# Optimization experiments

Hardware: AMD Instinct MI355X
Metric: run time of the kernel (lower is better)

Reference implementation:

```python
import jax, jax.numpy as jnp
import numpy as np

B, S, D_IN, D_OUT, H = 4, 2048, 1024, 1024, 16
HD = D_OUT // H

def setup_inputs() -> dict:
    key = jax.random.key(0)
    ks = jax.random.split(key, 6)
    s = 1.0 / np.sqrt(D_IN)
    return {
        "x": jax.random.normal(ks[0], (B, S, D_IN), dtype=jnp.float32),
        "Wq": jax.random.uniform(ks[1], (D_IN, D_OUT), jnp.float32, -s, s),
        "Wk": jax.random.uniform(ks[2], (D_IN, D_OUT), jnp.float32, -s, s),
        "Wv": jax.random.uniform(ks[3], (D_IN, D_OUT), jnp.float32, -s, s),
        "Wo": jax.random.uniform(ks[4], (D_OUT, D_OUT), jnp.float32, -s, s),
        "bo": jax.random.uniform(ks[5], (D_OUT,), jnp.float32, -s, s),
    }

def reference(x, Wq, Wk, Wv, Wo, bo):
    b, n, _ = x.shape
    # project and split heads: [b, h, n, hd]
    q = (x @ Wq).reshape(b, n, H, HD).transpose(0, 2, 1, 3)
    k = (x @ Wk).reshape(b, n, H, HD).transpose(0, 2, 1, 3)
    v = (x @ Wv).reshape(b, n, H, HD).transpose(0, 2, 1, 3)
    scores = jnp.einsum("bhqd,bhkd->bhqk", q, k) / np.sqrt(HD).astype(np.float32)
    causal = jnp.tril(jnp.ones((n, n), dtype=bool))
    scores = jnp.where(causal, scores, -jnp.inf)
    attn = jax.nn.softmax(scores, axis=-1)  # dropout p=0.0 -> identity
    ctx = jnp.einsum("bhqk,bhkd->bhqd", attn, v)
    ctx = ctx.transpose(0, 2, 1, 3).reshape(b, n, D_OUT)
    return ctx @ Wo + bo
```

## Files before the change

### kernel.cpp

```cpp
#include <hip/hip_runtime.h>
#include <stdint.h>

#define B_   4
#define S_   2048
#define DI   1024
#define DOUT 1024
#define NHD  16
#define HD   64

typedef __attribute__((ext_vector_type(8))) short short8;
typedef __attribute__((ext_vector_type(4))) float f32x4;
typedef __attribute__((ext_vector_type(16))) float f32x16;

__device__ __forceinline__ unsigned short f32_bf16(float f) {
  union { float f; unsigned u; } v; v.f = f;
  unsigned r = v.u + 0x7FFFu + ((v.u >> 16) & 1u);
  return (unsigned short)(r >> 16);
}

__device__ __forceinline__ unsigned cvt_pk_bf16(float a, float b) {
  unsigned r;
  asm("v_cvt_pk_bf16_f32 %0, %1, %2" : "=v"(r) : "v"(a), "v"(b));
  return r;
}

__device__ __forceinline__ void pl32swap(unsigned &dst, unsigned &src) {
  asm("v_permlane32_swap_b32 %0, %1" : "+v"(dst), "+v"(src));
}

__device__ __forceinline__ float max3f(float a, float b, float c) {
  float d;
  asm("v_max3_f32 %0, %1, %2, %3" : "=v"(d) : "v"(a), "v"(b), "v"(c));
  return d;
}

__device__ __forceinline__ void gl_lds16(const void* g, void* s) {
  __builtin_amdgcn_global_load_lds(
      (const __attribute__((address_space(1))) unsigned int*)g,
      (__attribute__((address_space(3))) unsigned int*)s, 16, 0, 0);
}

#define EXP2(x) __builtin_amdgcn_exp2f(x)

__global__ __launch_bounds__(256) void cvt_kernel(const float* __restrict__ src,
                                                  unsigned short* __restrict__ dst, int n4) {
  int i = blockIdx.x * blockDim.x + threadIdx.x;
  if (i < n4) {
    float4 v = ((const float4*)src)[i];
    ushort4 o;
    o.x = f32_bf16(v.x); o.y = f32_bf16(v.y); o.z = f32_bf16(v.z); o.w = f32_bf16(v.w);
    ((ushort4*)dst)[i] = o;
  }
}

__global__ __launch_bounds__(256) void wtrans4_kernel(
    const float* __restrict__ W0, const float* __restrict__ W1,
    const float* __restrict__ W2, const float* __restrict__ W3,
    unsigned short* __restrict__ T0, unsigned short* __restrict__ T1,
    unsigned short* __restrict__ T2, unsigned short* __restrict__ T3) {
  __shared__ __attribute__((aligned(16))) float tile[64][65];
  const int z = blockIdx.z;
  const float* W = z == 0 ? W0 : z == 1 ? W1 : z == 2 ? W2 : W3;
  unsigned short* Wt = z == 0 ? T0 : z == 1 ? T1 : z == 2 ? T2 : T3;
  const int k0 = blockIdx.y * 64;
  const int n0 = blockIdx.x * 64;
  const int tid = threadIdx.x;
#pragma unroll
  for (int i = 0; i < 4; i++) {
    int c = tid + i * 256;
    int r = c >> 4;
    int cc = (c & 15) * 4;
    float4 v = *(const float4*)(W + (size_t)(k0 + r) * DOUT + n0 + cc);
    tile[r][cc] = v.x; tile[r][cc + 1] = v.y; tile[r][cc + 2] = v.z; tile[r][cc + 3] = v.w;
  }
  __syncthreads();
#pragma unroll
  for (int i = 0; i < 4; i++) {
    int c = tid + i * 256;
    int r = c >> 4;
    int cc = (c & 15) * 4;
    ushort4 o;
    o.x = f32_bf16(tile[cc + 0][r]);
    o.y = f32_bf16(tile[cc + 1][r]);
    o.z = f32_bf16(tile[cc + 2][r]);
    o.w = f32_bf16(tile[cc + 3][r]);
    *(ushort4*)(Wt + (size_t)(n0 + r) * DI + k0 + cc) = o;
  }
}

__device__ __forceinline__ int cswz(int r, int c) {
  return r * 128 + ((((c >> 3) ^ ((r >> 3) & 15)) << 3) | (c & 7));
}

template <int MODE>
__global__ __launch_bounds__(256) void gemm_kernel(
    const unsigned short* __restrict__ A,
    const unsigned short* __restrict__ Bt,
    unsigned short* __restrict__ oQ,
    unsigned short* __restrict__ oK,
    unsigned short* __restrict__ oV,
    float* __restrict__ outF,
    const float* __restrict__ bias,
    int M, int N, int K) {
  __shared__ __attribute__((aligned(16))) unsigned short smem[16384];
  const int tid = threadIdx.x;
  const int lane = tid & 63;
  const int w = tid >> 6;
  const int wm = w >> 1, wn = w & 1;
  const int quad = lane >> 4, l16 = lane & 15;
  const int m0 = blockIdx.x * 128;
  const int n0 = blockIdx.y * 128;

  const int lr = lane >> 2;
  const int lc8 = (lane & 3) * 8;
  const unsigned short* gA0 = A + (size_t)(m0 + w * 32 + lr) * K + lc8;
  const unsigned short* gA1 = gA0 + (size_t)16 * K;
  const unsigned short* gB0 = Bt + (size_t)(n0 + w * 32 + lr) * K + lc8;
  const unsigned short* gB1 = gB0 + (size_t)16 * K;
  const int sA0o = (w * 2 + 0) * 512;
  const int sA1o = (w * 2 + 1) * 512;
  const int sB0o = 4096 + (w * 2 + 0) * 512;
  const int sB1o = 4096 + (w * 2 + 1) * 512;

  f32x4 acc[4][4] = {};

  gl_lds16(gA0, smem + sA0o);
  gl_lds16(gA1, smem + sA1o);
  gl_lds16(gB0, smem + sB0o);
  gl_lds16(gB1, smem + sB1o);
  __syncthreads();

  for (int k0 = 0; k0 < K; k0 += 32) {
    const int cb = ((k0 >> 5) & 1) << 13;
    const int nb = 8192 - cb;
    if (k0 + 32 < K) {
      gl_lds16(gA0 + k0 + 32, smem + nb + sA0o);
      gl_lds16(gA1 + k0 + 32, smem + nb + sA1o);
      gl_lds16(gB0 + k0 + 32, smem + nb + sB0o);
      gl_lds16(gB1 + k0 + 32, smem + nb + sB1o);
    }
    short8 af[4], bfr[4];
#pragma unroll
    for (int mi = 0; mi < 4; mi++)
      af[mi] = *(const short8*)(smem + cb + (wm * 64 + mi * 16 + l16) * 32 + quad * 8);
#pragma unroll
    for (int ni = 0; ni < 4; ni++)
      bfr[ni] = *(const short8*)(smem + cb + 4096 + (wn * 64 + ni * 16 + l16) * 32 + quad * 8);
#pragma unroll
    for (int mi = 0; mi < 4; mi++)
#pragma unroll
      for (int ni = 0; ni < 4; ni++)
        acc[mi][ni] = __builtin_amdgcn_mfma_f32_16x16x32_bf16(af[mi], bfr[ni], acc[mi][ni], 0, 0, 0);
    __syncthreads();
  }

  if (MODE == 0) {
    const int which = n0 >> 10;
    if (which == 2) {
#pragma unroll
      for (int mi = 0; mi < 4; mi++)
#pragma unroll
        for (int ni = 0; ni < 4; ni++)
#pragma unroll
          for (int r = 0; r < 4; r++)
            smem[cswz(wm * 64 + mi * 16 + quad * 4 + r, wn * 64 + ni * 16 + l16)] =
                f32_bf16(acc[mi][ni][r]);
      __syncthreads();
      const int b = m0 >> 11, sb = m0 & 2047;
#pragma unroll
      for (int i = 0; i < 8; i++) {
        int c = tid + i * 256;
        int cl = c >> 4;
        int sc = (c & 15) * 8;
        int col = n0 + cl;
        int hh = (col >> 6) & 15, hd = col & 63;
        union { unsigned short u[8]; uint4 v; } t;
#pragma unroll
        for (int j = 0; j < 8; j++) t.u[j] = smem[cswz(sc + j, cl)];
        *(uint4*)(oV + (((size_t)(b * NHD + hh)) * HD + hd) * S_ + sb + sc) = t.v;
      }
    } else {
      unsigned short* dst0 = which == 0 ? oQ : oK;
#pragma unroll
      for (int mi = 0; mi < 4; mi++)
#pragma unroll
        for (int ni = 0; ni < 4; ni++) {
          const int col = n0 + wn * 64 + ni * 16 + l16;
          const int hh = (col >> 6) & 15, hd = col & 63;
#pragma unroll
          for (int r = 0; r < 4; r++) {
            const int row = m0 + wm * 64 + mi * 16 + quad * 4 + r;
            int b = row >> 11, s = row & 2047;
            dst0[(((size_t)(b * NHD + hh)) * S_ + s) * HD + hd] = f32_bf16(acc[mi][ni][r]);
          }
        }
    }
  } else {
#pragma unroll
    for (int mi = 0; mi < 4; mi++)
#pragma unroll
      for (int ni = 0; ni < 4; ni++) {
        const int col = n0 + wn * 64 + ni * 16 + l16;
        float bv = bias[col];
#pragma unroll
        for (int r = 0; r < 4; r++) {
          const int row = m0 + wm * 64 + mi * 16 + quad * 4 + r;
          outF[(size_t)row * N + col] = acc[mi][ni][r] + bv;
        }
      }
  }
}

__global__ __launch_bounds__(256, 2) void attn_kernel(
    const unsigned short* __restrict__ Q,
    const unsigned short* __restrict__ Kmat,
    const unsigned short* __restrict__ Vt,
    unsigned short* __restrict__ ctx) {
  __shared__ __attribute__((aligned(16))) unsigned short Ks[2][64 * 64];
  __shared__ __attribute__((aligned(16))) unsigned short Vs[2][64 * 64];
  __shared__ __attribute__((aligned(16))) unsigned short PsT[128 * 72];

  const int tid = threadIdx.x;
  const int lane = tid & 63;
  const int w = tid >> 6;
  const int l32 = lane & 31;
  const int h = lane >> 5;

  const int bh = blockIdx.x & 63;
  const int jj = blockIdx.x >> 6;

  const unsigned short* Qh = Q + (size_t)bh * S_ * HD;
  const unsigned short* Kh = Kmat + (size_t)bh * S_ * HD;
  const unsigned short* Vh = Vt + (size_t)bh * HD * S_;

  const int sr = tid >> 2;
  const int jA = tid & 3, jB = jA + 4;
  const int sswA = sr * 64 + ((jA ^ (sr & 7)) << 3);
  const int sswB = sr * 64 + ((jB ^ (sr & 7)) << 3);
  const unsigned short* gKA = Kh + (size_t)sr * HD + jA * 8;
  const unsigned short* gKB = Kh + (size_t)sr * HD + jB * 8;
  const unsigned short* gVA = Vh + (size_t)sr * S_ + jA * 8;
  const unsigned short* gVB = Vh + (size_t)sr * S_ + jB * 8;
  const int swz = (l32 & 7);

  unsigned short* myP = PsT + (size_t)(w * 32) * 72;
  const float scl = 0.18033688f;
  const int b = bh >> 4, head = bh & 15;

  for (int ph = 0; ph < 2; ph++) {
    const int qc = (ph == 0) ? (jj * 8 + w) : (63 - jj * 8 - w);
    const int nt = (qc >> 1) + 1;
    const int ntmax = (ph == 0) ? (jj * 4 + 2) : (32 - jj * 4);
    const int qrow = qc * 32 + l32;

    short8 qf[4];
#pragma unroll
    for (int ks = 0; ks < 4; ks++)
      qf[ks] = *(const short8*)(Qh + (size_t)qrow * HD + ks * 16 + h * 8);

    uint4 kregA = *(const uint4*)gKA, kregB = *(const uint4*)gKB;
    uint4 vregA = *(const uint4*)gVA, vregB = *(const uint4*)gVB;
    *(uint4*)(&Ks[0][sswA]) = kregA;
    *(uint4*)(&Ks[0][sswB]) = kregB;
    *(uint4*)(&Vs[0][sswA]) = vregA;
    *(uint4*)(&Vs[0][sswB]) = vregB;
    __syncthreads();

    f32x16 oacc[2] = {};
    float m_run = -__builtin_inff();
    float l_run = 0.f;

    for (int kt = 0; kt < ntmax; kt++) {
      if (kt + 1 < ntmax) {
        kregA = *(const uint4*)(gKA + (size_t)(kt + 1) * 64 * HD);
        kregB = *(const uint4*)(gKB + (size_t)(kt + 1) * 64 * HD);
        vregA = *(const uint4*)(gVA + (size_t)(kt + 1) * 64);
        vregB = *(const uint4*)(gVB + (size_t)(kt + 1) * 64);
      }
      const unsigned short* Kb_ = Ks[kt & 1];
      const unsigned short* Vb_ = Vs[kt & 1];

      if (kt < nt) {
        const int k0 = kt * 64;
        f32x16 sacc[2] = {};
#pragma unroll
        for (int ks = 0; ks < 4; ks++)
#pragma unroll
          for (int mi = 0; mi < 2; mi++) {
            short8 kf = *(const short8*)(Kb_ + (mi * 32 + l32) * 64 + (((ks * 2 + h) ^ swz) << 3));
            sacc[mi] = __builtin_amdgcn_mfma_f32_32x32x16_bf16(kf, qf[ks], sacc[mi], 0, 0, 0);
          }

        if (kt == nt - 1) {
#pragma unroll
          for (int mi = 0; mi < 2; mi++)
#pragma unroll
            for (int e = 0; e < 16; e++) {
              int key = k0 + mi * 32 + (e & 3) + 8 * (e >> 2) + 4 * h;
              if (key > qrow) sacc[mi][e] = -__builtin_inff();
            }
        }
        float vmax = fmaxf(sacc[0][0], sacc[0][1]);
#pragma unroll
        for (int e = 2; e < 16; e += 2) vmax = max3f(vmax, sacc[0][e], sacc[0][e + 1]);
#pragma unroll
        for (int e = 0; e < 16; e += 2) vmax = max3f(vmax, sacc[1][e], sacc[1][e + 1]);
        vmax = fmaxf(vmax, __shfl_xor(vmax, 32));
        const float pm = vmax * scl;
        if (!__all(pm <= m_run + 8.f)) {
          const float mnew = fmaxf(m_run, pm);
          const float alpha = EXP2(m_run - mnew);
          m_run = mnew;
          l_run *= alpha;
#pragma unroll
          for (int mi = 0; mi < 2; mi++) oacc[mi] *= alpha;
        }

        float rs = 0.f;
#pragma unroll
        for (int mi = 0; mi < 2; mi++)
#pragma unroll
          for (int e = 0; e < 16; e++) {
            float p = EXP2(fmaf(sacc[mi][e], scl, -m_run));
            sacc[mi][e] = p;
            rs += p;
          }
        rs += __shfl_xor(rs, 32);
        l_run += rs;

        short8 pfr[4];
#pragma unroll
        for (int mi = 0; mi < 2; mi++) {
          unsigned w0 = cvt_pk_bf16(sacc[mi][0], sacc[mi][1]);
          unsigned w1 = cvt_pk_bf16(sacc[mi][2], sacc[mi][3]);
          unsigned w2 = cvt_pk_bf16(sacc[mi][4], sacc[mi][5]);
          unsigned w3 = cvt_pk_bf16(sacc[mi][6], sacc[mi][7]);
          pl32swap(w0, w2);
          pl32swap(w1, w3);
          union { unsigned u[4]; short8 s; } lo;
          lo.u[0] = w0; lo.u[1] = w1; lo.u[2] = w2; lo.u[3] = w3;
          pfr[2 * mi + 0] = lo.s;
          unsigned x0 = cvt_pk_bf16(sacc[mi][8], sacc[mi][9]);
          unsigned x1 = cvt_pk_bf16(sacc[mi][10], sacc[mi][11]);
          unsigned x2 = cvt_pk_bf16(sacc[mi][12], sacc[mi][13]);
          unsigned x3 = cvt_pk_bf16(sacc[mi][14], sacc[mi][15]);
          pl32swap(x0, x2);
          pl32swap(x1, x3);
          union { unsigned u[4]; short8 s; } hi;
          hi.u[0] = x0; hi.u[1] = x1; hi.u[2] = x2; hi.u[3] = x3;
          pfr[2 * mi + 1] = hi.s;
        }

#pragma unroll
        for (int ks2 = 0; ks2 < 4; ks2++) {
#pragma unroll
          for (int mi2 = 0; mi2 < 2; mi2++) {
            short8 vf = *(const short8*)(Vb_ + (mi2 * 32 + l32) * 64 + (((ks2 * 2 + h) ^ swz) << 3));
            oacc[mi2] = __builtin_amdgcn_mfma_f32_32x32x16_bf16(vf, pfr[ks2], oacc[mi2], 0, 0, 0);
          }
        }
      }

      if (kt + 1 < ntmax) {
        *(uint4*)(&Ks[(kt + 1) & 1][sswA]) = kregA;
        *(uint4*)(&Ks[(kt + 1) & 1][sswB]) = kregB;
        *(uint4*)(&Vs[(kt + 1) & 1][sswA]) = vregA;
        *(uint4*)(&Vs[(kt + 1) & 1][sswB]) = vregB;
      }
      __syncthreads();
    }

    const float inv = 1.f / l_run;
#pragma unroll
    for (int mi2 = 0; mi2 < 2; mi2++)
#pragma unroll
      for (int g = 0; g < 4; g++) {
        uint2 pk;
        pk.x = cvt_pk_bf16(oacc[mi2][4 * g + 0] * inv, oacc[mi2][4 * g + 1] * inv);
        pk.y = cvt_pk_bf16(oacc[mi2][4 * g + 2] * inv, oacc[mi2][4 * g + 3] * inv);
        *(uint2*)(myP + l32 * 72 + mi2 * 32 + g * 8 + h * 4) = pk;
      }
#pragma unroll
    for (int p = 0; p < 4; p++) {
      int r = p * 8 + (lane >> 3);
      int c = (lane & 7) * 8;
      uint4 vv = *(const uint4*)(myP + r * 72 + c);
      *(uint4*)(ctx + ((size_t)(b * S_ + qc * 32 + r)) * DOUT + head * 64 + c) = vv;
    }
  }
}

extern "C" void kernel_launch(void* const* d_in, const int* in_sizes, int n_in,
                              void* d_out, int out_size, void* d_ws, size_t ws_size,
                              hipStream_t stream) {
  const float* x  = (const float*)d_in[0];
  const float* Wq = (const float*)d_in[1];
  const float* Wk = (const float*)d_in[2];
  const float* Wv = (const float*)d_in[3];
  const float* Wo = (const float*)d_in[4];
  const float* bo = (const float*)d_in[5];
  float* out = (float*)d_out;
  char* ws = (char*)d_ws;

  const size_t MB = 1024 * 1024;
  unsigned short* Wqt = (unsigned short*)(ws + 0 * MB);
  unsigned short* Wkt = (unsigned short*)(ws + 2 * MB);
  unsigned short* Wvt = (unsigned short*)(ws + 4 * MB);
  unsigned short* Wot = (unsigned short*)(ws + 6 * MB);
  unsigned short* xb  = (unsigned short*)(ws + 8 * MB);
  unsigned short* Qb  = (unsigned short*)(ws + 24 * MB);
  unsigned short* Kb  = (unsigned short*)(ws + 40 * MB);
  unsigned short* Vtb = (unsigned short*)(ws + 72 * MB);
  unsigned short* ctxb = xb;

  cvt_kernel<<<8192, 256, 0, stream>>>(x, xb, 2097152);
  wtrans4_kernel<<<dim3(16, 16, 4), 256, 0, stream>>>(Wq, Wk, Wv, Wo, Wqt, Wkt, Wvt, Wot);
  gemm_kernel<0><<<dim3(64, 24), 256, 0, stream>>>(xb, Wqt, Qb, Kb, Vtb, nullptr, nullptr,
                                                   8192, 3072, 1024);
  attn_kernel<<<512, 256, 0, stream>>>(Qb, Kb, Vtb, ctxb);
  gemm_kernel<1><<<dim3(64, 8), 256, 0, stream>>>(ctxb, Wot, nullptr, nullptr, nullptr, out, bo,
                                                  8192, 1024, 1024);
}
```

Baseline: 238.9 us.

## Switch projection GEMM to 32x32x16 MFMA with two-tile-ahead prefetch pipeline

The projection and output GEMM kernel now uses 32x32x16 bf16 MFMA tiles (2x2 per wave) in place of 16x16x32 tiles (4x4 per wave). This cuts the number of LDS fragment reads per MFMA FLOP. The K loop is restructured to keep two tiles in flight, with explicit vmcnt/lgkmcnt waits and raw s_barrier, so global-to-LDS loads overlap with compute. The epilogues are remapped to the 32x32 accumulator layout. The risk lies in correctness of the hand-placed waitcnt and barrier ordering, and the double buffer is reused right after fragments are read.

Result: slower. 246.0 us (+3.0%).

```diff
diff --git a/kernel.cpp b/kernel.cpp
--- a/kernel.cpp
+++ b/kernel.cpp
@@ -107,7 +107,8 @@
   const int lane = tid & 63;
   const int w = tid >> 6;
   const int wm = w >> 1, wn = w & 1;
-  const int quad = lane >> 4, l16 = lane & 15;
+  const int l32 = lane & 31;
+  const int h = lane >> 5;
   const int m0 = blockIdx.x * 128;
   const int n0 = blockIdx.y * 128;
 
@@ -122,49 +123,68 @@
   const int sB0o = 4096 + (w * 2 + 0) * 512;
   const int sB1o = 4096 + (w * 2 + 1) * 512;
 
-  f32x4 acc[4][4] = {};
-
-  gl_lds16(gA0, smem + sA0o);
-  gl_lds16(gA1, smem + sA1o);
-  gl_lds16(gB0, smem + sB0o);
-  gl_lds16(gB1, smem + sB1o);
-  __syncthreads();
-
-  for (int k0 = 0; k0 < K; k0 += 32) {
-    const int cb = ((k0 >> 5) & 1) << 13;
-    const int nb = 8192 - cb;
-    if (k0 + 32 < K) {
-      gl_lds16(gA0 + k0 + 32, smem + nb + sA0o);
-      gl_lds16(gA1 + k0 + 32, smem + nb + sA1o);
-      gl_lds16(gB0 + k0 + 32, smem + nb + sB0o);
-      gl_lds16(gB1 + k0 + 32, smem + nb + sB1o);
+  f32x16 acc[2][2] = {};
+
+  const int nt = K >> 5;
+
+#define STAGE_T(t, bufS)                                \
+  do {                                                  \
+    gl_lds16(gA0 + (t) * 32, smem + (bufS) + sA0o);     \
+    gl_lds16(gA1 + (t) * 32, smem + (bufS) + sA1o);     \
+    gl_lds16(gB0 + (t) * 32, smem + (bufS) + sB0o);     \
+    gl_lds16(gB1 + (t) * 32, smem + (bufS) + sB1o);     \
+  } while (0)
+
+  STAGE_T(0, 0);
+  STAGE_T(1, 8192);
+  asm volatile("s_waitcnt vmcnt(4)" ::: "memory");
+  __builtin_amdgcn_s_barrier();
+
+  for (int it = 0; it < nt; ++it) {
+    const int cb = (it & 1) << 13;
+    short8 af[2][2], bf[2][2];
+#pragma unroll
+    for (int mi = 0; mi < 2; mi++)
+#pragma unroll
+      for (int ks = 0; ks < 2; ks++)
+        af[mi][ks] = *(const short8*)(smem + cb + (wm * 64 + mi * 32 + l32) * 32 + (ks * 2 + h) * 8);
+#pragma unroll
+    for (int ni = 0; ni < 2; ni++)
+#pragma unroll
+      for (int ks = 0; ks < 2; ks++)
+        bf[ni][ks] = *(const short8*)(smem + cb + 4096 + (wn * 64 + ni * 32 + l32) * 32 + (ks * 2 + h) * 8);
+    asm volatile("s_waitcnt lgkmcnt(0)" ::: "memory");
+    __builtin_amdgcn_s_barrier();
+    if (it + 2 < nt) STAGE_T(it + 2, cb);
+#pragma unroll
+    for (int mi = 0; mi < 2; mi++)
+#pragma unroll
+      for (int ni = 0; ni < 2; ni++) {
+        acc[mi][ni] = __builtin_amdgcn_mfma_f32_32x32x16_bf16(af[mi][0], bf[ni][0], acc[mi][ni], 0, 0, 0);
+        acc[mi][ni] = __builtin_amdgcn_mfma_f32_32x32x16_bf16(af[mi][1], bf[ni][1], acc[mi][ni], 0, 0, 0);
+      }
+    if (it + 2 < nt) {
+      asm volatile("s_waitcnt vmcnt(4)" ::: "memory");
+    } else {
+      asm volatile("s_waitcnt vmcnt(0)" ::: "memory");
     }
-    short8 af[4], bfr[4];
-#pragma unroll
-    for (int mi = 0; mi < 4; mi++)
-      af[mi] = *(const short8*)(smem + cb + (wm * 64 + mi * 16 + l16) * 32 + quad * 8);
-#pragma unroll
-    for (int ni = 0; ni < 4; ni++)
-      bfr[ni] = *(const short8*)(smem + cb + 4096 + (wn * 64 + ni * 16 + l16) * 32 + quad * 8);
-#pragma unroll
-    for (int mi = 0; mi < 4; mi++)
-#pragma unroll
-      for (int ni = 0; ni < 4; ni++)
-        acc[mi][ni] = __builtin_amdgcn_mfma_f32_16x16x32_bf16(af[mi], bfr[ni], acc[mi][ni], 0, 0, 0);
-    __syncthreads();
-  }
+    __builtin_amdgcn_s_barrier();
+  }
+#undef STAGE_T
 
   if (MODE == 0) {
     const int which = n0 >> 10;
     if (which == 2) {
 #pragma unroll
-      for (int mi = 0; mi < 4; mi++)
-#pragma unroll
-        for (int ni = 0; ni < 4; ni++)
-#pragma unroll
-          for (int r = 0; r < 4; r++)
-            smem[cswz(wm * 64 + mi * 16 + quad * 4 + r, wn * 64 + ni * 16 + l16)] =
-                f32_bf16(acc[mi][ni][r]);
+      for (int mi = 0; mi < 2; mi++)
+#pragma unroll
+        for (int ni = 0; ni < 2; ni++)
+#pragma unroll
+          for (int e = 0; e < 16; e++) {
+            const int rw = (e & 3) + 8 * (e >> 2) + 4 * h;
+            smem[cswz(wm * 64 + mi * 32 + rw, wn * 64 + ni * 32 + l32)] =
+                f32_bf16(acc[mi][ni][e]);
+          }
       __syncthreads();
       const int b = m0 >> 11, sb = m0 & 2047;
 #pragma unroll
@@ -182,30 +202,30 @@
     } else {
       unsigned short* dst0 = which == 0 ? oQ : oK;
 #pragma unroll
-      for (int mi = 0; mi < 4; mi++)
-#pragma unroll
-        for (int ni = 0; ni < 4; ni++) {
-          const int col = n0 + wn * 64 + ni * 16 + l16;
+      for (int mi = 0; mi < 2; mi++)
+#pragma unroll
+        for (int ni = 0; ni < 2; ni++) {
+          const int col = n0 + wn * 64 + ni * 32 + l32;
           const int hh = (col >> 6) & 15, hd = col & 63;
 #pragma unroll
-          for (int r = 0; r < 4; r++) {
-            const int row = m0 + wm * 64 + mi * 16 + quad * 4 + r;
+          for (int e = 0; e < 16; e++) {
+            const int row = m0 + wm * 64 + mi * 32 + (e & 3) + 8 * (e >> 2) + 4 * h;
             int b = row >> 11, s = row & 2047;
-            dst0[(((size_t)(b * NHD + hh)) * S_ + s) * HD + hd] = f32_bf16(acc[mi][ni][r]);
+            dst0[(((size_t)(b * NHD + hh)) * S_ + s) * HD + hd] = f32_bf16(acc[mi][ni][e]);
           }
         }
     }
   } else {
 #pragma unroll
-    for (int mi = 0; mi < 4; mi++)
-#pragma unroll
-      for (int ni = 0; ni < 4; ni++) {
-        const int col = n0 + wn * 64 + ni * 16 + l16;
+    for (int mi = 0; mi < 2; mi++)
+#pragma unroll
+      for (int ni = 0; ni < 2; ni++) {
+        const int col = n0 + wn * 64 + ni * 32 + l32;
         float bv = bias[col];
 #pragma unroll
-        for (int r = 0; r < 4; r++) {
-          const int row = m0 + wm * 64 + mi * 16 + quad * 4 + r;
-          outF[(size_t)row * N + col] = acc[mi][ni][r] + bv;
+        for (int e = 0; e < 16; e++) {
+          const int row = m0 + wm * 64 + mi * 32 + (e & 3) + 8 * (e >> 2) + 4 * h;
+          outF[(size_t)row * N + col] = acc[mi][ni][e] + bv;
         }
       }
   }
```

## Process 64 query rows per wave in attention and remap blocks across XCDs

Applied to the files above, without the earlier changes.

Each attention wave now handles two 32-row query chunks (64 rows) against every K/V tile loaded into shared memory. This doubles the reuse of each K/V fragment read from LDS per MFMA and halves the number of blocks to 256. Block indices in both the GEMM and attention kernels are also remapped so that neighbouring tiles and heads land on the same XCD, aiming for better L2 locality. The trade-offs are roughly twice the accumulator and Q-fragment registers, which may hurt occupancy, and fewer blocks than before with coarser causal load balancing.

Result: slower. 256.4 us (+7.3%).

```diff
diff --git a/kernel.cpp b/kernel.cpp
--- a/kernel.cpp
+++ b/kernel.cpp
@@ -108,8 +108,14 @@
   const int w = tid >> 6;
   const int wm = w >> 1, wn = w & 1;
   const int quad = lane >> 4, l16 = lane & 15;
-  const int m0 = blockIdx.x * 128;
-  const int n0 = blockIdx.y * 128;
+
+  const int bid = blockIdx.y * 64 + blockIdx.x;
+  const int xcd = bid & 7;
+  const int rr = bid >> 3;
+  const int bx = xcd * 8 + (rr & 7);
+  const int by = rr >> 3;
+  const int m0 = bx * 128;
+  const int n0 = by * 128;
 
   const int lr = lane >> 2;
   const int lc8 = (lane & 3) * 8;
@@ -176,7 +182,7 @@
         int hh = (col >> 6) & 15, hd = col & 63;
         union { unsigned short u[8]; uint4 v; } t;
 #pragma unroll
-        for (int j = 0; j < 8; j++) t.u[j] = smem[cswz(sc + j, cl)];
+        for (int jx = 0; jx < 8; jx++) t.u[jx] = smem[cswz(sc + jx, cl)];
         *(uint4*)(oV + (((size_t)(b * NHD + hh)) * HD + hd) * S_ + sb + sc) = t.v;
       }
     } else {
@@ -226,8 +232,10 @@
   const int l32 = lane & 31;
   const int h = lane >> 5;
 
-  const int bh = blockIdx.x & 63;
-  const int jj = blockIdx.x >> 6;
+  const int bid = blockIdx.x;
+  const int bh = (bid & 7) * 8 + ((bid >> 3) & 7);
+  const int j = bid >> 6;
+  const int slot = 4 * j + w;
 
   const unsigned short* Qh = Q + (size_t)bh * S_ * HD;
   const unsigned short* Kh = Kmat + (size_t)bh * S_ * HD;
@@ -248,15 +256,17 @@
   const int b = bh >> 4, head = bh & 15;
 
   for (int ph = 0; ph < 2; ph++) {
-    const int qc = (ph == 0) ? (jj * 8 + w) : (63 - jj * 8 - w);
-    const int nt = (qc >> 1) + 1;
-    const int ntmax = (ph == 0) ? (jj * 4 + 2) : (32 - jj * 4);
-    const int qrow = qc * 32 + l32;
-
-    short8 qf[4];
-#pragma unroll
-    for (int ks = 0; ks < 4; ks++)
-      qf[ks] = *(const short8*)(Qh + (size_t)qrow * HD + ks * 16 + h * 8);
+    const int qp = (ph == 0) ? slot : (31 - slot);
+    const int nt = qp + 1;
+    const int ntmax = (ph == 0) ? (4 * j + 4) : (32 - 4 * j);
+    const int qr0 = qp * 64;
+
+    short8 qf[2][4];
+#pragma unroll
+    for (int c = 0; c < 2; c++)
+#pragma unroll
+      for (int ks = 0; ks < 4; ks++)
+        qf[c][ks] = *(const short8*)(Qh + (size_t)(qr0 + c * 32 + l32) * HD + ks * 16 + h * 8);
 
     uint4 kregA = *(const uint4*)gKA, kregB = *(const uint4*)gKB;
     uint4 vregA = *(const uint4*)gVA, vregB = *(const uint4*)gVB;
@@ -266,9 +276,9 @@
     *(uint4*)(&Vs[0][sswB]) = vregB;
     __syncthreads();
 
-    f32x16 oacc[2] = {};
-    float m_run = -__builtin_inff();
-    float l_run = 0.f;
+    f32x16 oacc[2][2] = {};
+    float m_run[2] = {-__builtin_inff(), -__builtin_inff()};
+    float l_run[2] = {0.f, 0.f};
 
     for (int kt = 0; kt < ntmax; kt++) {
       if (kt + 1 < ntmax) {
@@ -282,83 +292,92 @@
 
       if (kt < nt) {
         const int k0 = kt * 64;
-        f32x16 sacc[2] = {};
+        f32x16 sacc[2][2] = {};
 #pragma unroll
         for (int ks = 0; ks < 4; ks++)
 #pragma unroll
           for (int mi = 0; mi < 2; mi++) {
             short8 kf = *(const short8*)(Kb_ + (mi * 32 + l32) * 64 + (((ks * 2 + h) ^ swz) << 3));
-            sacc[mi] = __builtin_amdgcn_mfma_f32_32x32x16_bf16(kf, qf[ks], sacc[mi], 0, 0, 0);
+            sacc[0][mi] = __builtin_amdgcn_mfma_f32_32x32x16_bf16(kf, qf[0][ks], sacc[0][mi], 0, 0, 0);
+            sacc[1][mi] = __builtin_amdgcn_mfma_f32_32x32x16_bf16(kf, qf[1][ks], sacc[1][mi], 0, 0, 0);
           }
 
         if (kt == nt - 1) {
 #pragma unroll
+          for (int c = 0; c < 2; c++) {
+            const int qrow = qr0 + c * 32 + l32;
+#pragma unroll
+            for (int mi = 0; mi < 2; mi++)
+#pragma unroll
+              for (int e = 0; e < 16; e++) {
+                int key = k0 + mi * 32 + (e & 3) + 8 * (e >> 2) + 4 * h;
+                if (key > qrow) sacc[c][mi][e] = -__builtin_inff();
+              }
+          }
+        }
+
+        short8 pfr[2][4];
+#pragma unroll
+        for (int c = 0; c < 2; c++) {
+          float vmax = fmaxf(sacc[c][0][0], sacc[c][0][1]);
+#pragma unroll
+          for (int e = 2; e < 16; e += 2) vmax = max3f(vmax, sacc[c][0][e], sacc[c][0][e + 1]);
+#pragma unroll
+          for (int e = 0; e < 16; e += 2) vmax = max3f(vmax, sacc[c][1][e], sacc[c][1][e + 1]);
+          vmax = fmaxf(vmax, __shfl_xor(vmax, 32));
+          const float pm = vmax * scl;
+          if (!__all(pm <= m_run[c] + 8.f)) {
+            const float mnew = fmaxf(m_run[c], pm);
+            const float alpha = EXP2(m_run[c] - mnew);
+            m_run[c] = mnew;
+            l_run[c] *= alpha;
+#pragma unroll
+            for (int mi = 0; mi < 2; mi++) oacc[c][mi] *= alpha;
+          }
+
+          float rs = 0.f;
+#pragma unroll
           for (int mi = 0; mi < 2; mi++)
 #pragma unroll
             for (int e = 0; e < 16; e++) {
-              int key = k0 + mi * 32 + (e & 3) + 8 * (e >> 2) + 4 * h;
-              if (key > qrow) sacc[mi][e] = -__builtin_inff();
+              float p = EXP2(fmaf(sacc[c][mi][e], scl, -m_run[c]));
+              sacc[c][mi][e] = p;
+              rs += p;
             }
+          rs += __shfl_xor(rs, 32);
+          l_run[c] += rs;
+
+#pragma unroll
+          for (int mi = 0; mi < 2; mi++) {
+            unsigned w0 = cvt_pk_bf16(sacc[c][mi][0], sacc[c][mi][1]);
+            unsigned w1 = cvt_pk_bf16(sacc[c][mi][2], sacc[c][mi][3]);
+            unsigned w2 = cvt_pk_bf16(sacc[c][mi][4], sacc[c][mi][5]);
+            unsigned w3 = cvt_pk_bf16(sacc[c][mi][6], sacc[c][mi][7]);
+            pl32swap(w0, w2);
+            pl32swap(w1, w3);
+            union { unsigned u[4]; short8 s; } lo;
+            lo.u[0] = w0; lo.u[1] = w1; lo.u[2] = w2; lo.u[3] = w3;
+            pfr[c][2 * mi + 0] = lo.s;
+            unsigned x0 = cvt_pk_bf16(sacc[c][mi][8], sacc[c][mi][9]);
+            unsigned x1 = cvt_pk_bf16(sacc[c][mi][10], sacc[c][mi][11]);
+            unsigned x2 = cvt_pk_bf16(sacc[c][mi][12], sacc[c][mi][13]);
+            unsigned x3 = cvt_pk_bf16(sacc[c][mi][14], sacc[c][mi][15]);
+            pl32swap(x0, x2);
+            pl32swap(x1, x3);
+            union { unsigned u[4]; short8 s; } hi;
+            hi.u[0] = x0; hi.u[1] = x1; hi.u[2] = x2; hi.u[3] = x3;
+            pfr[c][2 * mi + 1] = hi.s;
+          }
         }
-        float vmax = fmaxf(sacc[0][0], sacc[0][1]);
-#pragma unroll
-        for (int e = 2; e < 16; e += 2) vmax = max3f(vmax, sacc[0][e], sacc[0][e + 1]);
-#pragma unroll
-        for (int e = 0; e < 16; e += 2) vmax = max3f(vmax, sacc[1][e], sacc[1][e + 1]);
-        vmax = fmaxf(vmax, __shfl_xor(vmax, 32));
-        const float pm = vmax * scl;
-        if (!__all(pm <= m_run + 8.f)) {
-          const float mnew = fmaxf(m_run, pm);
-          const float alpha = EXP2(m_run - mnew);
-          m_run = mnew;
-          l_run *= alpha;
-#pragma unroll
-          for (int mi = 0; mi < 2; mi++) oacc[mi] *= alpha;
-        }
-
-        float rs = 0.f;
-#pragma unroll
-        for (int mi = 0; mi < 2; mi++)
-#pragma unroll
-          for (int e = 0; e < 16; e++) {
-            float p = EXP2(fmaf(sacc[mi][e], scl, -m_run));
-            sacc[mi][e] = p;
-            rs += p;
-          }
-        rs += __shfl_xor(rs, 32);
-        l_run += rs;
-
-        short8 pfr[4];
-#pragma unroll
-        for (int mi = 0; mi < 2; mi++) {
-          unsigned w0 = cvt_pk_bf16(sacc[mi][0], sacc[mi][1]);
-          unsigned w1 = cvt_pk_bf16(sacc[mi][2], sacc[mi][3]);
-          unsigned w2 = cvt_pk_bf16(sacc[mi][4], sacc[mi][5]);
-          unsigned w3 = cvt_pk_bf16(sacc[mi][6], sacc[mi][7]);
-          pl32swap(w0, w2);
-          pl32swap(w1, w3);
-          union { unsigned u[4]; short8 s; } lo;
-          lo.u[0] = w0; lo.u[1] = w1; lo.u[2] = w2; lo.u[3] = w3;
-          pfr[2 * mi + 0] = lo.s;
-          unsigned x0 = cvt_pk_bf16(sacc[mi][8], sacc[mi][9]);
-          unsigned x1 = cvt_pk_bf16(sacc[mi][10], sacc[mi][11]);
-          unsigned x2 = cvt_pk_bf16(sacc[mi][12], sacc[mi][13]);
-          unsigned x3 = cvt_pk_bf16(sacc[mi][14], sacc[mi][15]);
-          pl32swap(x0, x2);
-          pl32swap(x1, x3);
-          union { unsigned u[4]; short8 s; } hi;
-          hi.u[0] = x0; hi.u[1] = x1; hi.u[2] = x2; hi.u[3] = x3;
-          pfr[2 * mi + 1] = hi.s;
-        }
-
-#pragma unroll
-        for (int ks2 = 0; ks2 < 4; ks2++) {
+
+#pragma unroll
+        for (int ks2 = 0; ks2 < 4; ks2++)
 #pragma unroll
           for (int mi2 = 0; mi2 < 2; mi2++) {
             short8 vf = *(const short8*)(Vb_ + (mi2 * 32 + l32) * 64 + (((ks2 * 2 + h) ^ swz) << 3));
-            oacc[mi2] = __builtin_amdgcn_mfma_f32_32x32x16_bf16(vf, pfr[ks2], oacc[mi2], 0, 0, 0);
-          }
-        }
+            oacc[0][mi2] = __builtin_amdgcn_mfma_f32_32x32x16_bf16(vf, pfr[0][ks2], oacc[0][mi2], 0, 0, 0);
+            oacc[1][mi2] = __builtin_amdgcn_mfma_f32_32x32x16_bf16(vf, pfr[1][ks2], oacc[1][mi2], 0, 0, 0);
+          }
       }
 
       if (kt + 1 < ntmax) {
@@ -370,22 +389,26 @@
       __syncthreads();
     }
 
-    const float inv = 1.f / l_run;
-#pragma unroll
-    for (int mi2 = 0; mi2 < 2; mi2++)
-#pragma unroll
-      for (int g = 0; g < 4; g++) {
-        uint2 pk;
-        pk.x = cvt_pk_bf16(oacc[mi2][4 * g + 0] * inv, oacc[mi2][4 * g + 1] * inv);
-        pk.y = cvt_pk_bf16(oacc[mi2][4 * g + 2] * inv, oacc[mi2][4 * g + 3] * inv);
-        *(uint2*)(myP + l32 * 72 + mi2 * 32 + g * 8 + h * 4) = pk;
-      }
-#pragma unroll
-    for (int p = 0; p < 4; p++) {
-      int r = p * 8 + (lane >> 3);
-      int c = (lane & 7) * 8;
-      uint4 vv = *(const uint4*)(myP + r * 72 + c);
-      *(uint4*)(ctx + ((size_t)(b * S_ + qc * 32 + r)) * DOUT + head * 64 + c) = vv;
+#pragma unroll
+    for (int c = 0; c < 2; c++) {
+      const float inv = 1.f / l_run[c];
+#pragma unroll
+      for (int mi2 = 0; mi2 < 2; mi2++)
+#pragma unroll
+        for (int g = 0; g < 4; g++) {
+          uint2 pk;
+          pk.x = cvt_pk_bf16(oacc[c][mi2][4 * g + 0] * inv, oacc[c][mi2][4 * g + 1] * inv);
+          pk.y = cvt_pk_bf16(oacc[c][mi2][4 * g + 2] * inv, oacc[c][mi2][4 * g + 3] * inv);
+          *(uint2*)(myP + l32 * 72 + mi2 * 32 + g * 8 + h * 4) = pk;
+        }
+      const int qcc = qp * 2 + c;
+#pragma unroll
+      for (int p = 0; p < 4; p++) {
+        int r = p * 8 + (lane >> 3);
+        int cc = (lane & 7) * 8;
+        uint4 vv = *(const uint4*)(myP + r * 72 + cc);
+        *(uint4*)(ctx + ((size_t)(b * S_ + qcc * 32 + r)) * DOUT + head * 64 + cc) = vv;
+      }
     }
   }
 }
@@ -417,7 +440,7 @@
   wtrans4_kernel<<<dim3(16, 16, 4), 256, 0, stream>>>(Wq, Wk, Wv, Wo, Wqt, Wkt, Wvt, Wot);
   gemm_kernel<0><<<dim3(64, 24), 256, 0, stream>>>(xb, Wqt, Qb, Kb, Vtb, nullptr, nullptr,
                                                    8192, 3072, 1024);
-  attn_kernel<<<512, 256, 0, stream>>>(Qb, Kb, Vtb, ctxb);
+  attn_kernel<<<256, 256, 0, stream>>>(Qb, Kb, Vtb, ctxb);
   gemm_kernel<1><<<dim3(64, 8), 256, 0, stream>>>(ctxb, Wot, nullptr, nullptr, nullptr, out, bo,
                                                   8192, 1024, 1024);
 }
```

## Alias attention P buffer onto K/V LDS, raise occupancy, add XCD-aware block remapping

Applied to the files above, without the earlier changes.

The attention kernel's separate K, V and P shared buffers are merged into one 32KB array, with the P staging area aliased onto the K buffers. This lowers LDS use per block so the launch bound can go from 2 to 4 blocks per CU. A barrier is added after the epilogue so the next phase cannot overwrite P while it is still being read. Both the GEMM and attention block indices are remapped so blocks sharing data land on the same XCD, aiming for better L2 reuse. The risk is register pressure from the tighter launch bound, which could cause spills.

Result: slower. 260.1 us (+8.9%).

```diff
diff --git a/kernel.cpp b/kernel.cpp
--- a/kernel.cpp
+++ b/kernel.cpp
@@ -108,8 +108,14 @@
   const int w = tid >> 6;
   const int wm = w >> 1, wn = w & 1;
   const int quad = lane >> 4, l16 = lane & 15;
-  const int m0 = blockIdx.x * 128;
-  const int n0 = blockIdx.y * 128;
+
+  const int bid = blockIdx.y * 64 + blockIdx.x;
+  const int xcd = bid & 7;
+  const int rr = bid >> 3;
+  const int bx = xcd * 8 + (rr & 7);
+  const int by = rr >> 3;
+  const int m0 = bx * 128;
+  const int n0 = by * 128;
 
   const int lr = lane >> 2;
   const int lc8 = (lane & 3) * 8;
@@ -176,7 +182,7 @@
         int hh = (col >> 6) & 15, hd = col & 63;
         union { unsigned short u[8]; uint4 v; } t;
 #pragma unroll
-        for (int j = 0; j < 8; j++) t.u[j] = smem[cswz(sc + j, cl)];
+        for (int jx = 0; jx < 8; jx++) t.u[jx] = smem[cswz(sc + jx, cl)];
         *(uint4*)(oV + (((size_t)(b * NHD + hh)) * HD + hd) * S_ + sb + sc) = t.v;
       }
     } else {
@@ -211,14 +217,12 @@
   }
 }
 
-__global__ __launch_bounds__(256, 2) void attn_kernel(
+__global__ __launch_bounds__(256, 4) void attn_kernel(
     const unsigned short* __restrict__ Q,
     const unsigned short* __restrict__ Kmat,
     const unsigned short* __restrict__ Vt,
     unsigned short* __restrict__ ctx) {
-  __shared__ __attribute__((aligned(16))) unsigned short Ks[2][64 * 64];
-  __shared__ __attribute__((aligned(16))) unsigned short Vs[2][64 * 64];
-  __shared__ __attribute__((aligned(16))) unsigned short PsT[128 * 72];
+  __shared__ __attribute__((aligned(16))) unsigned short smem[16384];
 
   const int tid = threadIdx.x;
   const int lane = tid & 63;
@@ -226,8 +230,9 @@
   const int l32 = lane & 31;
   const int h = lane >> 5;
 
-  const int bh = blockIdx.x & 63;
-  const int jj = blockIdx.x >> 6;
+  const int bid = blockIdx.x;
+  const int bh = (bid & 7) * 8 + ((bid >> 3) & 7);
+  const int jj = bid >> 6;
 
   const unsigned short* Qh = Q + (size_t)bh * S_ * HD;
   const unsigned short* Kh = Kmat + (size_t)bh * S_ * HD;
@@ -243,7 +248,7 @@
   const unsigned short* gVB = Vh + (size_t)sr * S_ + jB * 8;
   const int swz = (l32 & 7);
 
-  unsigned short* myP = PsT + (size_t)(w * 32) * 72;
+  unsigned short* myP = smem + (size_t)(w * 32) * 72;
   const float scl = 0.18033688f;
   const int b = bh >> 4, head = bh & 15;
 
@@ -260,10 +265,10 @@
 
     uint4 kregA = *(const uint4*)gKA, kregB = *(const uint4*)gKB;
     uint4 vregA = *(const uint4*)gVA, vregB = *(const uint4*)gVB;
-    *(uint4*)(&Ks[0][sswA]) = kregA;
-    *(uint4*)(&Ks[0][sswB]) = kregB;
-    *(uint4*)(&Vs[0][sswA]) = vregA;
-    *(uint4*)(&Vs[0][sswB]) = vregB;
+    *(uint4*)(smem + sswA) = kregA;
+    *(uint4*)(smem + sswB) = kregB;
+    *(uint4*)(smem + 8192 + sswA) = vregA;
+    *(uint4*)(smem + 8192 + sswB) = vregB;
     __syncthreads();
 
     f32x16 oacc[2] = {};
@@ -277,8 +282,8 @@
         vregA = *(const uint4*)(gVA + (size_t)(kt + 1) * 64);
         vregB = *(const uint4*)(gVB + (size_t)(kt + 1) * 64);
       }
-      const unsigned short* Kb_ = Ks[kt & 1];
-      const unsigned short* Vb_ = Vs[kt & 1];
+      const unsigned short* Kb_ = smem + ((kt & 1) << 12);
+      const unsigned short* Vb_ = smem + 8192 + ((kt & 1) << 12);
 
       if (kt < nt) {
         const int k0 = kt * 64;
@@ -362,10 +367,10 @@
       }
 
       if (kt + 1 < ntmax) {
-        *(uint4*)(&Ks[(kt + 1) & 1][sswA]) = kregA;
-        *(uint4*)(&Ks[(kt + 1) & 1][sswB]) = kregB;
-        *(uint4*)(&Vs[(kt + 1) & 1][sswA]) = vregA;
-        *(uint4*)(&Vs[(kt + 1) & 1][sswB]) = vregB;
+        *(uint4*)(smem + ((~kt & 1) << 12) + sswA) = kregA;
+        *(uint4*)(smem + ((~kt & 1) << 12) + sswB) = kregB;
+        *(uint4*)(smem + 8192 + ((~kt & 1) << 12) + sswA) = vregA;
+        *(uint4*)(smem + 8192 + ((~kt & 1) << 12) + sswB) = vregB;
       }
       __syncthreads();
     }
@@ -387,6 +392,7 @@
       uint4 vv = *(const uint4*)(myP + r * 72 + c);
       *(uint4*)(ctx + ((size_t)(b * S_ + qc * 32 + r)) * DOUT + head * 64 + c) = vv;
     }
+    __syncthreads();
   }
 }
 
```
